# Optimization experiments

Hardware: AMD Instinct MI355X
Metric: run time of the kernel (lower is better)

Reference implementation:

```python
import jax, jax.numpy as jnp
import numpy as np

K = 3          # kernel_size (local window)
PAD = 1        # padding = (K-1)//2 -> 'same' output size
GROUPS = 8
C_OUT = 64


def _unfold3d(x, k):
    """x: [B,C,Dp,Hp,Wp] -> [B,C,D,H,W,kd,kh,kw] sliding windows (stride 1)."""
    B, C, Dp, Hp, Wp = x.shape
    D, H, W = Dp - k + 1, Hp - k + 1, Wp - k + 1
    idx_d = jnp.arange(D)[:, None] + jnp.arange(k)[None, :]
    idx_h = jnp.arange(H)[:, None] + jnp.arange(k)[None, :]
    idx_w = jnp.arange(W)[:, None] + jnp.arange(k)[None, :]
    x = x[:, :, idx_d]              # [B,C,D,kd,Hp,Wp]
    x = x[:, :, :, :, idx_h]        # [B,C,D,kd,H,kh,Wp]
    x = x[:, :, :, :, :, :, idx_w]  # [B,C,D,kd,H,kh,W,kw]
    return jnp.transpose(x, (0, 1, 2, 4, 6, 3, 5, 7))


def setup_inputs() -> dict:
    key = jax.random.key(0)
    ks = jax.random.split(key, 7)
    B, Cin, D, H, W = 1, 64, 16, 64, 64
    c3 = C_OUT // 3                 # 21
    rest = C_OUT - 2 * c3           # 22
    fan_out_scale = np.sqrt(2.0 / C_OUT)  # kaiming_normal fan_out, relu
    x = jax.random.normal(ks[0], (B, Cin, D, H, W), dtype=jnp.float32)
    w_q = jax.random.normal(ks[1], (C_OUT, Cin), dtype=jnp.float32) * fan_out_scale
    w_k = jax.random.normal(ks[2], (C_OUT, Cin), dtype=jnp.float32) * fan_out_scale
    w_v = jax.random.normal(ks[3], (C_OUT, Cin), dtype=jnp.float32) * fan_out_scale
    rel_d = jax.random.normal(ks[4], (c3, 1, 1, 1, K, 1, 1), dtype=jnp.float32)
    rel_h = jax.random.normal(ks[5], (c3, 1, 1, 1, 1, K, 1), dtype=jnp.float32)
    rel_w = jax.random.normal(ks[6], (rest, 1, 1, 1, 1, 1, K), dtype=jnp.float32)
    return {"x": x, "w_q": w_q, "w_k": w_k, "w_v": w_v,
            "rel_d": rel_d, "rel_h": rel_h, "rel_w": rel_w}


def reference(x, w_q, w_k, w_v, rel_d, rel_h, rel_w):
    B, Cin, D, H, W = x.shape
    cg = C_OUT // GROUPS
    c3 = C_OUT // 3
    # 1x1x1 convs (bias=False): plain channel mixing. conv(pad(x)) == pad(conv(x)).
    q = jnp.einsum('oc,bcdhw->bodhw', w_q, x)
    k = jnp.einsum('oc,bcdhw->bodhw', w_k, x)
    v = jnp.einsum('oc,bcdhw->bodhw', w_v, x)
    pad = [(0, 0), (0, 0), (PAD, PAD), (PAD, PAD), (PAD, PAD)]
    k = jnp.pad(k, pad)
    v = jnp.pad(v, pad)
    k_win = _unfold3d(k, K)   # [B,Co,D,H,W,kd,kh,kw]
    v_win = _unfold3d(v, K)
    # split relative position bias across channel thirds
    k_win = jnp.concatenate([
        k_win[:, :c3] + rel_d,
        k_win[:, c3:2 * c3] + rel_h,
        k_win[:, 2 * c3:] + rel_w,
    ], axis=1)
    Kv = K * K * K
    k_win = k_win.reshape(B, GROUPS, cg, D, H, W, Kv)
    v_win = v_win.reshape(B, GROUPS, cg, D, H, W, Kv)
    qg = q.reshape(B, GROUPS, cg, D, H, W, 1)
    attn = jax.nn.softmax(qg * k_win, axis=-1)
    out = jnp.einsum('bncdhwk,bncdhwk->bncdhw', attn, v_win)
    return out.reshape(B, C_OUT, D, H, W)
```

## Files before the change

### kernel.cpp

```cpp
#include <hip/hip_runtime.h>

#define SP    65536
#define DD    16
#define HH    64
#define WW    64
#define CIN   64
#define COUT  64

#define LOG2E 1.44269504f


typedef __attribute__((ext_vector_type(8))) short bf16x8;
typedef __attribute__((ext_vector_type(4))) float f32x4;

__device__ __forceinline__ unsigned short f2bf(float f) {
    const unsigned u = __float_as_uint(f);
    return (unsigned short)((u + 0x7FFFu + ((u >> 16) & 1u)) >> 16);
}
__device__ __forceinline__ float bf2f(unsigned short h) {
    return __uint_as_float((unsigned)h << 16);
}

__global__ __launch_bounds__(256) void proj(const float* __restrict__ x,
                                            const float* __restrict__ wq,
                                            const float* __restrict__ wk,
                                            const float* __restrict__ wv,
                                            float* __restrict__ q,
                                            float* __restrict__ k,
                                            float* __restrict__ v) {
    __shared__ __align__(16) unsigned short xh [64][72];
    __shared__ __align__(16) unsigned short xlo[64][72];
    __shared__ __align__(16) unsigned short wh [64][72];
    __shared__ __align__(16) unsigned short wlo[64][72];

    const int t  = threadIdx.x;
    const int p0 = blockIdx.x * 64;
    const int m  = blockIdx.y;

    const float* __restrict__ wsel = (m == 0) ? wq : (m == 1) ? wk : wv;
    float* __restrict__       osel = (m == 0) ? q  : (m == 1) ? k  : v;

#pragma unroll
    for (int i = 0; i < 2; ++i) {
        const int f  = t + 256 * i;
        const int c2 = (f >> 4) * 2;
        const int jj = f & 15;
        const float4 a = *(const float4*)(x + c2 * SP + p0 + jj * 4);
        const float4 b = *(const float4*)(x + (c2 + 1) * SP + p0 + jj * 4);
        const float* af = (const float*)&a;
        const float* bf = (const float*)&b;
#pragma unroll
        for (int e = 0; e < 4; ++e) {
            const int j = jj * 4 + e;
            const unsigned short ah = f2bf(af[e]);
            const unsigned short bh = f2bf(bf[e]);
            const unsigned short al = f2bf(af[e] - bf2f(ah));
            const unsigned short bl = f2bf(bf[e] - bf2f(bh));
            *(unsigned*)&xh [j][c2] = (unsigned)ah | ((unsigned)bh << 16);
            *(unsigned*)&xlo[j][c2] = (unsigned)al | ((unsigned)bl << 16);
        }
    }
#pragma unroll
    for (int i = 0; i < 4; ++i) {
        const int f  = t + 256 * i;
        const int o  = f >> 4;
        const int jj = f & 15;
        const float4 w4 = *(const float4*)(wsel + o * CIN + jj * 4);
        const float* wf = (const float*)&w4;
        unsigned short h0 = f2bf(wf[0]), h1 = f2bf(wf[1]);
        unsigned short h2 = f2bf(wf[2]), h3 = f2bf(wf[3]);
        unsigned short l0 = f2bf(wf[0] - bf2f(h0)), l1 = f2bf(wf[1] - bf2f(h1));
        unsigned short l2 = f2bf(wf[2] - bf2f(h2)), l3 = f2bf(wf[3] - bf2f(h3));
        *(uint2*)&wh [o][jj * 4] = make_uint2((unsigned)h0 | ((unsigned)h1 << 16),
                                              (unsigned)h2 | ((unsigned)h3 << 16));
        *(uint2*)&wlo[o][jj * 4] = make_uint2((unsigned)l0 | ((unsigned)l1 << 16),
                                              (unsigned)l2 | ((unsigned)l3 << 16));
    }
    __syncthreads();

    const int lane  = t & 63;
    const int wid   = t >> 6;
    const int lo16  = lane & 15;
    const int lg    = lane >> 4;
    const int otile = wid * 16;

    const bf16x8 Ah0 = *(const bf16x8*)&wh [otile + lo16][lg * 8];
    const bf16x8 Ah1 = *(const bf16x8*)&wh [otile + lo16][32 + lg * 8];
    const bf16x8 Al0 = *(const bf16x8*)&wlo[otile + lo16][lg * 8];
    const bf16x8 Al1 = *(const bf16x8*)&wlo[otile + lo16][32 + lg * 8];

    const float scale = (m == 0) ? LOG2E : 1.f;

#pragma unroll
    for (int jt = 0; jt < 4; ++jt) {
        const int jr = jt * 16 + lo16;
        const bf16x8 Bh0 = *(const bf16x8*)&xh [jr][lg * 8];
        const bf16x8 Bl0 = *(const bf16x8*)&xlo[jr][lg * 8];
        const bf16x8 Bh1 = *(const bf16x8*)&xh [jr][32 + lg * 8];
        const bf16x8 Bl1 = *(const bf16x8*)&xlo[jr][32 + lg * 8];
        f32x4 hh = {0.f, 0.f, 0.f, 0.f};
        f32x4 hl = {0.f, 0.f, 0.f, 0.f};
        f32x4 lh = {0.f, 0.f, 0.f, 0.f};
        hh = __builtin_amdgcn_mfma_f32_16x16x32_bf16(Ah0, Bh0, hh, 0, 0, 0);
        hl = __builtin_amdgcn_mfma_f32_16x16x32_bf16(Ah0, Bl0, hl, 0, 0, 0);
        lh = __builtin_amdgcn_mfma_f32_16x16x32_bf16(Al0, Bh0, lh, 0, 0, 0);
        hh = __builtin_amdgcn_mfma_f32_16x16x32_bf16(Ah1, Bh1, hh, 0, 0, 0);
        hl = __builtin_amdgcn_mfma_f32_16x16x32_bf16(Ah1, Bl1, hl, 0, 0, 0);
        lh = __builtin_amdgcn_mfma_f32_16x16x32_bf16(Al1, Bh1, lh, 0, 0, 0);
        float* op = osel + (otile + lg * 4) * SP + p0 + jt * 16 + lo16;
#pragma unroll
        for (int r = 0; r < 4; ++r)
            op[r * SP] = (hh[r] + hl[r] + lh[r]) * scale;
    }
}

__device__ __forceinline__ float dpp_shr1(float x) {
    return __int_as_float(__builtin_amdgcn_mov_dpp(__float_as_int(x), 0x111, 0xf, 0xf, true));
}
__device__ __forceinline__ float dpp_shl1(float x) {
    return __int_as_float(__builtin_amdgcn_mov_dpp(__float_as_int(x), 0x101, 0xf, 0xf, true));
}

template<int AXIS>
__device__ __forceinline__ void attn_walk(const float* __restrict__ kc,
                                          const float* __restrict__ vc,
                                          const float (&ql)[4],
                                          float r0, float r1, float r2,
                                          int wg, int dabs, int habs,
                                          float (&s)[4], float (&a)[4]) {
#pragma unroll 1
    for (int kd = 0; kd < 3; ++kd) {
        const float rdd = (kd == 0) ? r0 : (kd == 1) ? r1 : r2;
        const int dpg   = dabs - 1 + kd;
        const bool okd  = (unsigned)dpg < (unsigned)DD;
#pragma unroll
        for (int kh = 0; kh < 3; ++kh) {
            const float rkh = (kh == 0) ? r0 : (kh == 1) ? r1 : r2;
            const float rr  = (AXIS == 0) ? rdd : rkh;
            const int hpg   = habs - 1 + kh;
            const bool ok   = okd && ((unsigned)hpg < (unsigned)HH);
            const int off   = ok ? ((dpg * HH + hpg) * WW + wg * 4) : 0;
            float4 km = *(const float4*)(kc + off);
            float4 vm = *(const float4*)(vc + off);
            if (!ok) {
                km = make_float4(0.f, 0.f, 0.f, 0.f);
                vm = make_float4(0.f, 0.f, 0.f, 0.f);
            }
            const float kl = dpp_shr1(km.w), kr = dpp_shl1(km.x);
            const float vl = dpp_shr1(vm.w), vr = dpp_shl1(vm.x);
            float krow[6] = { kl, km.x, km.y, km.z, km.w, kr };
            const float vrow[6] = { vl, vm.x, vm.y, vm.z, vm.w, vr };
            if (AXIS != 2) {
#pragma unroll
                for (int j = 0; j < 6; ++j) krow[j] += rr;
            }
#pragma unroll
            for (int wi = 0; wi < 4; ++wi) {
                const float qv = ql[wi];
#pragma unroll
                for (int kw = 0; kw < 3; ++kw) {
                    const float arg = (AXIS == 2)
                                    ? (krow[wi + kw] + ((kw == 0) ? r0 : (kw == 1) ? r1 : r2))
                                    : krow[wi + kw];
                    const float e = __builtin_amdgcn_exp2f(qv * arg);
                    s[wi] += e;
                    a[wi] = fmaf(e, vrow[wi + kw], a[wi]);
                }
            }
        }
    }
}

__global__ __launch_bounds__(256) void attn(const float* __restrict__ kbuf,
                                            const float* __restrict__ vbuf,
                                            const float* __restrict__ qbuf,
                                            const float* __restrict__ rel_d,
                                            const float* __restrict__ rel_h,
                                            const float* __restrict__ rel_w,
                                            float* __restrict__ out) {
    const int dt = blockIdx.x;
    const int ht = blockIdx.y;
    const int o  = blockIdx.z;

    const int d0 = dt * 4;
    const int h0 = ht * 4;
    const int t  = threadIdx.x;

    const float* __restrict__ kc = kbuf + o * SP;
    const float* __restrict__ vc = vbuf + o * SP;

    const int wg = t & 15;
    const int hl = (t >> 4) & 3;
    const int dl = t >> 6;

    const int dabs = d0 + dl;
    const int habs = h0 + hl;

    float ql[4];
    {
        const float4 q4 = *(const float4*)(qbuf + o * SP + (dabs * HH + habs) * WW + wg * 4);
        ql[0] = q4.x; ql[1] = q4.y;
        ql[2] = q4.z; ql[3] = q4.w;
    }

    float s[4] = {};
    float a[4] = {};

    if (o < 21) {
        attn_walk<0>(kc, vc, ql, rel_d[o * 3], rel_d[o * 3 + 1], rel_d[o * 3 + 2],
                     wg, dabs, habs, s, a);
    } else if (o < 42) {
        const int b = o - 21;
        attn_walk<1>(kc, vc, ql, rel_h[b * 3], rel_h[b * 3 + 1], rel_h[b * 3 + 2],
                     wg, dabs, habs, s, a);
    } else {
        const int b = o - 42;
        attn_walk<2>(kc, vc, ql, rel_w[b * 3], rel_w[b * 3 + 1], rel_w[b * 3 + 2],
                     wg, dabs, habs, s, a);
    }

    float4 ov;
    ov.x = a[0] * __builtin_amdgcn_rcpf(s[0]);
    ov.y = a[1] * __builtin_amdgcn_rcpf(s[1]);
    ov.z = a[2] * __builtin_amdgcn_rcpf(s[2]);
    ov.w = a[3] * __builtin_amdgcn_rcpf(s[3]);
    *(float4*)(out + o * SP + (dabs * HH + habs) * WW + wg * 4) = ov;
}

extern "C" void kernel_launch(void* const* d_in, const int* in_sizes, int n_in,
                              void* d_out, int out_size, void* d_ws, size_t ws_size,
                              hipStream_t stream) {
    const float* x     = (const float*)d_in[0];
    const float* w_q   = (const float*)d_in[1];
    const float* w_k   = (const float*)d_in[2];
    const float* w_v   = (const float*)d_in[3];
    const float* rel_d = (const float*)d_in[4];
    const float* rel_h = (const float*)d_in[5];
    const float* rel_w = (const float*)d_in[6];
    float* out = (float*)d_out;

    float* ws = (float*)d_ws;
    float* q  = ws;
    float* k  = ws + (size_t)COUT * SP;
    float* v  = ws + 2 * (size_t)COUT * SP;

    proj<<<dim3(SP / 64, 3), 256, 0, stream>>>(x, w_q, w_k, w_v, q, k, v);
    attn<<<dim3(4, 16, 64), 256, 0, stream>>>(k, v, q, rel_d, rel_h, rel_w, out);
}
```

Baseline: 115.7 us.

## Precompute bf16 hi/lo split of x and weights in a separate kernel

Adds a splitk kernel that converts x into transposed bf16 high/low arrays and the three weight matrices into bf16 high/low pairs once, writing them to workspace. The proj kernel then reads those pre-split operands straight from global memory into MFMA registers, with no LDS staging, no per-block conversion and no barrier. Previously every one of the three projection blocks per tile redid the x split. The cost is an extra kernel launch plus a write and re-read of the bf16 x copies (about the same bytes as the fp32 x), and uncoalesced-ish 16-byte row loads in proj.

After: 136.5 us. 17.9% more time.

```diff
diff --git a/kernel.cpp b/kernel.cpp
--- a/kernel.cpp
+++ b/kernel.cpp
@@ -21,25 +21,44 @@
     return __uint_as_float((unsigned)h << 16);
 }
 
-__global__ __launch_bounds__(256) void proj(const float* __restrict__ x,
-                                            const float* __restrict__ wq,
-                                            const float* __restrict__ wk,
-                                            const float* __restrict__ wv,
-                                            float* __restrict__ q,
-                                            float* __restrict__ k,
-                                            float* __restrict__ v) {
-    __shared__ __align__(16) unsigned short xh [64][72];
-    __shared__ __align__(16) unsigned short xlo[64][72];
-    __shared__ __align__(16) unsigned short wh [64][72];
-    __shared__ __align__(16) unsigned short wlo[64][72];
-
-    const int t  = threadIdx.x;
-    const int p0 = blockIdx.x * 64;
-    const int m  = blockIdx.y;
-
-    const float* __restrict__ wsel = (m == 0) ? wq : (m == 1) ? wk : wv;
-    float* __restrict__       osel = (m == 0) ? q  : (m == 1) ? k  : v;
-
+__global__ __launch_bounds__(256) void splitk(const float* __restrict__ x,
+                                              const float* __restrict__ wq,
+                                              const float* __restrict__ wk,
+                                              const float* __restrict__ wv,
+                                              unsigned short* __restrict__ xhT,
+                                              unsigned short* __restrict__ xlT,
+                                              unsigned short* __restrict__ wsp) {
+    const int bid = blockIdx.x;
+    const int t   = threadIdx.x;
+
+    if (bid >= 1024) {
+        const int m = bid - 1024;
+        const float* __restrict__ wsel = (m == 0) ? wq : (m == 1) ? wk : wv;
+        unsigned short* dh = wsp + m * 8192;
+        unsigned short* dl = dh + 4096;
+#pragma unroll
+        for (int i = 0; i < 4; ++i) {
+            const int f = t + 256 * i;
+            const float4 w4 = *(const float4*)(wsel + f * 4);
+            const float* wf = (const float*)&w4;
+            unsigned short h[4], l[4];
+#pragma unroll
+            for (int e = 0; e < 4; ++e) {
+                h[e] = f2bf(wf[e]);
+                l[e] = f2bf(wf[e] - bf2f(h[e]));
+            }
+            *(uint2*)(dh + f * 4) = make_uint2((unsigned)h[0] | ((unsigned)h[1] << 16),
+                                               (unsigned)h[2] | ((unsigned)h[3] << 16));
+            *(uint2*)(dl + f * 4) = make_uint2((unsigned)l[0] | ((unsigned)l[1] << 16),
+                                               (unsigned)l[2] | ((unsigned)l[3] << 16));
+        }
+        return;
+    }
+
+    __shared__ __align__(16) unsigned short sh[64][72];
+    __shared__ __align__(16) unsigned short sl[64][72];
+
+    const int p0 = bid * 64;
 #pragma unroll
     for (int i = 0; i < 2; ++i) {
         const int f  = t + 256 * i;
@@ -56,48 +75,58 @@
             const unsigned short bh = f2bf(bf[e]);
             const unsigned short al = f2bf(af[e] - bf2f(ah));
             const unsigned short bl = f2bf(bf[e] - bf2f(bh));
-            *(unsigned*)&xh [j][c2] = (unsigned)ah | ((unsigned)bh << 16);
-            *(unsigned*)&xlo[j][c2] = (unsigned)al | ((unsigned)bl << 16);
+            *(unsigned*)&sh[j][c2] = (unsigned)ah | ((unsigned)bh << 16);
+            *(unsigned*)&sl[j][c2] = (unsigned)al | ((unsigned)bl << 16);
         }
     }
+    __syncthreads();
+
 #pragma unroll
     for (int i = 0; i < 4; ++i) {
-        const int f  = t + 256 * i;
-        const int o  = f >> 4;
-        const int jj = f & 15;
-        const float4 w4 = *(const float4*)(wsel + o * CIN + jj * 4);
-        const float* wf = (const float*)&w4;
-        unsigned short h0 = f2bf(wf[0]), h1 = f2bf(wf[1]);
-        unsigned short h2 = f2bf(wf[2]), h3 = f2bf(wf[3]);
-        unsigned short l0 = f2bf(wf[0] - bf2f(h0)), l1 = f2bf(wf[1] - bf2f(h1));
-        unsigned short l2 = f2bf(wf[2] - bf2f(h2)), l3 = f2bf(wf[3] - bf2f(h3));
-        *(uint2*)&wh [o][jj * 4] = make_uint2((unsigned)h0 | ((unsigned)h1 << 16),
-                                              (unsigned)h2 | ((unsigned)h3 << 16));
-        *(uint2*)&wlo[o][jj * 4] = make_uint2((unsigned)l0 | ((unsigned)l1 << 16),
-                                              (unsigned)l2 | ((unsigned)l3 << 16));
-    }
-    __syncthreads();
-
-    const int lane  = t & 63;
-    const int wid   = t >> 6;
+        const int idx = t + 256 * i;
+        const int row = idx >> 4;
+        const int seg = idx & 15;
+        const uint2 hv = *(const uint2*)&sh[row][seg * 4];
+        const uint2 lv = *(const uint2*)&sl[row][seg * 4];
+        *(uint2*)(xhT + (size_t)(p0 + row) * 64 + seg * 4) = hv;
+        *(uint2*)(xlT + (size_t)(p0 + row) * 64 + seg * 4) = lv;
+    }
+}
+
+__global__ __launch_bounds__(256) void proj(const unsigned short* __restrict__ xhT,
+                                            const unsigned short* __restrict__ xlT,
+                                            const unsigned short* __restrict__ wsp,
+                                            float* __restrict__ q,
+                                            float* __restrict__ k,
+                                            float* __restrict__ v) {
+    const int p0 = blockIdx.x * 64;
+    const int m  = blockIdx.y;
+    float* __restrict__ osel = (m == 0) ? q : (m == 1) ? k : v;
+    const unsigned short* wh = wsp + m * 8192;
+    const unsigned short* wl = wh + 4096;
+
+    const int lane  = threadIdx.x & 63;
+    const int wid   = threadIdx.x >> 6;
     const int lo16  = lane & 15;
     const int lg    = lane >> 4;
     const int otile = wid * 16;
 
-    const bf16x8 Ah0 = *(const bf16x8*)&wh [otile + lo16][lg * 8];
-    const bf16x8 Ah1 = *(const bf16x8*)&wh [otile + lo16][32 + lg * 8];
-    const bf16x8 Al0 = *(const bf16x8*)&wlo[otile + lo16][lg * 8];
-    const bf16x8 Al1 = *(const bf16x8*)&wlo[otile + lo16][32 + lg * 8];
+    const bf16x8 Ah0 = *(const bf16x8*)(wh + (otile + lo16) * 64 + lg * 8);
+    const bf16x8 Ah1 = *(const bf16x8*)(wh + (otile + lo16) * 64 + 32 + lg * 8);
+    const bf16x8 Al0 = *(const bf16x8*)(wl + (otile + lo16) * 64 + lg * 8);
+    const bf16x8 Al1 = *(const bf16x8*)(wl + (otile + lo16) * 64 + 32 + lg * 8);
 
     const float scale = (m == 0) ? LOG2E : 1.f;
 
-#pragma unroll
+#pragma unroll 2
     for (int jt = 0; jt < 4; ++jt) {
         const int jr = jt * 16 + lo16;
-        const bf16x8 Bh0 = *(const bf16x8*)&xh [jr][lg * 8];
-        const bf16x8 Bl0 = *(const bf16x8*)&xlo[jr][lg * 8];
-        const bf16x8 Bh1 = *(const bf16x8*)&xh [jr][32 + lg * 8];
-        const bf16x8 Bl1 = *(const bf16x8*)&xlo[jr][32 + lg * 8];
+        const unsigned short* xrh = xhT + (size_t)(p0 + jr) * 64;
+        const unsigned short* xrl = xlT + (size_t)(p0 + jr) * 64;
+        const bf16x8 Bh0 = *(const bf16x8*)(xrh + lg * 8);
+        const bf16x8 Bl0 = *(const bf16x8*)(xrl + lg * 8);
+        const bf16x8 Bh1 = *(const bf16x8*)(xrh + 32 + lg * 8);
+        const bf16x8 Bl1 = *(const bf16x8*)(xrl + 32 + lg * 8);
         f32x4 hh = {0.f, 0.f, 0.f, 0.f};
         f32x4 hl = {0.f, 0.f, 0.f, 0.f};
         f32x4 lh = {0.f, 0.f, 0.f, 0.f};
@@ -243,7 +272,11 @@
     float* q  = ws;
     float* k  = ws + (size_t)COUT * SP;
     float* v  = ws + 2 * (size_t)COUT * SP;
-
-    proj<<<dim3(SP / 64, 3), 256, 0, stream>>>(x, w_q, w_k, w_v, q, k, v);
+    unsigned short* xhT = (unsigned short*)(ws + 3 * (size_t)COUT * SP);
+    unsigned short* xlT = xhT + (size_t)CIN * SP;
+    unsigned short* wsp = xlT + (size_t)CIN * SP;
+
+    splitk<<<dim3(1027), 256, 0, stream>>>(x, w_q, w_k, w_v, xhT, xlT, wsp);
+    proj<<<dim3(SP / 64, 3), 256, 0, stream>>>(xhT, xlT, wsp, q, k, v);
     attn<<<dim3(4, 16, 64), 256, 0, stream>>>(k, v, q, rel_d, rel_h, rel_w, out);
 }
```

## Fuse Q/K/V projections per block and precompute bf16 weight splits

Applied to the files above, without the earlier changes.

Adds a tiny kernel that splits the three weight matrices into bf16 hi/lo parts once into workspace. The projection kernel then runs one block per 64-position tile and computes Q, K and V together, so each x tile is loaded and split into bf16 hi/lo once instead of three times. The cost is one extra launch and more registers for the three weight fragment sets, which may reduce occupancy.

New measurement: 117.6 us. No clear change (+1.6%).

```diff
diff --git a/kernel.cpp b/kernel.cpp
--- a/kernel.cpp
+++ b/kernel.cpp
@@ -21,24 +21,43 @@
     return __uint_as_float((unsigned)h << 16);
 }
 
+__global__ __launch_bounds__(256) void splitw(const float* __restrict__ wq,
+                                              const float* __restrict__ wk,
+                                              const float* __restrict__ wv,
+                                              unsigned short* __restrict__ wsp) {
+    const int m = blockIdx.x;
+    const int t = threadIdx.x;
+    const float* __restrict__ wsel = (m == 0) ? wq : (m == 1) ? wk : wv;
+    unsigned short* dh = wsp + m * 8192;
+    unsigned short* dl = dh + 4096;
+#pragma unroll
+    for (int i = 0; i < 4; ++i) {
+        const int f = t + 256 * i;
+        const float4 w4 = *(const float4*)(wsel + f * 4);
+        const float* wf = (const float*)&w4;
+        unsigned short h[4], l[4];
+#pragma unroll
+        for (int e = 0; e < 4; ++e) {
+            h[e] = f2bf(wf[e]);
+            l[e] = f2bf(wf[e] - bf2f(h[e]));
+        }
+        *(uint2*)(dh + f * 4) = make_uint2((unsigned)h[0] | ((unsigned)h[1] << 16),
+                                           (unsigned)h[2] | ((unsigned)h[3] << 16));
+        *(uint2*)(dl + f * 4) = make_uint2((unsigned)l[0] | ((unsigned)l[1] << 16),
+                                           (unsigned)l[2] | ((unsigned)l[3] << 16));
+    }
+}
+
 __global__ __launch_bounds__(256) void proj(const float* __restrict__ x,
-                                            const float* __restrict__ wq,
-                                            const float* __restrict__ wk,
-                                            const float* __restrict__ wv,
+                                            const unsigned short* __restrict__ wsp,
                                             float* __restrict__ q,
                                             float* __restrict__ k,
                                             float* __restrict__ v) {
     __shared__ __align__(16) unsigned short xh [64][72];
     __shared__ __align__(16) unsigned short xlo[64][72];
-    __shared__ __align__(16) unsigned short wh [64][72];
-    __shared__ __align__(16) unsigned short wlo[64][72];
 
     const int t  = threadIdx.x;
     const int p0 = blockIdx.x * 64;
-    const int m  = blockIdx.y;
-
-    const float* __restrict__ wsel = (m == 0) ? wq : (m == 1) ? wk : wv;
-    float* __restrict__       osel = (m == 0) ? q  : (m == 1) ? k  : v;
 
 #pragma unroll
     for (int i = 0; i < 2; ++i) {
@@ -60,23 +79,6 @@
             *(unsigned*)&xlo[j][c2] = (unsigned)al | ((unsigned)bl << 16);
         }
     }
-#pragma unroll
-    for (int i = 0; i < 4; ++i) {
-        const int f  = t + 256 * i;
-        const int o  = f >> 4;
-        const int jj = f & 15;
-        const float4 w4 = *(const float4*)(wsel + o * CIN + jj * 4);
-        const float* wf = (const float*)&w4;
-        unsigned short h0 = f2bf(wf[0]), h1 = f2bf(wf[1]);
-        unsigned short h2 = f2bf(wf[2]), h3 = f2bf(wf[3]);
-        unsigned short l0 = f2bf(wf[0] - bf2f(h0)), l1 = f2bf(wf[1] - bf2f(h1));
-        unsigned short l2 = f2bf(wf[2] - bf2f(h2)), l3 = f2bf(wf[3] - bf2f(h3));
-        *(uint2*)&wh [o][jj * 4] = make_uint2((unsigned)h0 | ((unsigned)h1 << 16),
-                                              (unsigned)h2 | ((unsigned)h3 << 16));
-        *(uint2*)&wlo[o][jj * 4] = make_uint2((unsigned)l0 | ((unsigned)l1 << 16),
-                                              (unsigned)l2 | ((unsigned)l3 << 16));
-    }
-    __syncthreads();
 
     const int lane  = t & 63;
     const int wid   = t >> 6;
@@ -84,33 +86,45 @@
     const int lg    = lane >> 4;
     const int otile = wid * 16;
 
-    const bf16x8 Ah0 = *(const bf16x8*)&wh [otile + lo16][lg * 8];
-    const bf16x8 Ah1 = *(const bf16x8*)&wh [otile + lo16][32 + lg * 8];
-    const bf16x8 Al0 = *(const bf16x8*)&wlo[otile + lo16][lg * 8];
-    const bf16x8 Al1 = *(const bf16x8*)&wlo[otile + lo16][32 + lg * 8];
-
-    const float scale = (m == 0) ? LOG2E : 1.f;
-
-#pragma unroll
+    bf16x8 Ah[3][2], Al[3][2];
+#pragma unroll
+    for (int m = 0; m < 3; ++m) {
+        const unsigned short* wh = wsp + m * 8192;
+        const unsigned short* wl = wh + 4096;
+#pragma unroll
+        for (int ch = 0; ch < 2; ++ch) {
+            Ah[m][ch] = *(const bf16x8*)(wh + (otile + lo16) * 64 + ch * 32 + lg * 8);
+            Al[m][ch] = *(const bf16x8*)(wl + (otile + lo16) * 64 + ch * 32 + lg * 8);
+        }
+    }
+    __syncthreads();
+
+    float* outp[3] = { q, k, v };
+    const float scl[3] = { LOG2E, 1.f, 1.f };
+
+#pragma unroll 2
     for (int jt = 0; jt < 4; ++jt) {
         const int jr = jt * 16 + lo16;
         const bf16x8 Bh0 = *(const bf16x8*)&xh [jr][lg * 8];
         const bf16x8 Bl0 = *(const bf16x8*)&xlo[jr][lg * 8];
         const bf16x8 Bh1 = *(const bf16x8*)&xh [jr][32 + lg * 8];
         const bf16x8 Bl1 = *(const bf16x8*)&xlo[jr][32 + lg * 8];
-        f32x4 hh = {0.f, 0.f, 0.f, 0.f};
-        f32x4 hl = {0.f, 0.f, 0.f, 0.f};
-        f32x4 lh = {0.f, 0.f, 0.f, 0.f};
-        hh = __builtin_amdgcn_mfma_f32_16x16x32_bf16(Ah0, Bh0, hh, 0, 0, 0);
-        hl = __builtin_amdgcn_mfma_f32_16x16x32_bf16(Ah0, Bl0, hl, 0, 0, 0);
-        lh = __builtin_amdgcn_mfma_f32_16x16x32_bf16(Al0, Bh0, lh, 0, 0, 0);
-        hh = __builtin_amdgcn_mfma_f32_16x16x32_bf16(Ah1, Bh1, hh, 0, 0, 0);
-        hl = __builtin_amdgcn_mfma_f32_16x16x32_bf16(Ah1, Bl1, hl, 0, 0, 0);
-        lh = __builtin_amdgcn_mfma_f32_16x16x32_bf16(Al1, Bh1, lh, 0, 0, 0);
-        float* op = osel + (otile + lg * 4) * SP + p0 + jt * 16 + lo16;
-#pragma unroll
-        for (int r = 0; r < 4; ++r)
-            op[r * SP] = (hh[r] + hl[r] + lh[r]) * scale;
+#pragma unroll
+        for (int m = 0; m < 3; ++m) {
+            f32x4 hh = {0.f, 0.f, 0.f, 0.f};
+            f32x4 hl = {0.f, 0.f, 0.f, 0.f};
+            f32x4 lh = {0.f, 0.f, 0.f, 0.f};
+            hh = __builtin_amdgcn_mfma_f32_16x16x32_bf16(Ah[m][0], Bh0, hh, 0, 0, 0);
+            hl = __builtin_amdgcn_mfma_f32_16x16x32_bf16(Ah[m][0], Bl0, hl, 0, 0, 0);
+            lh = __builtin_amdgcn_mfma_f32_16x16x32_bf16(Al[m][0], Bh0, lh, 0, 0, 0);
+            hh = __builtin_amdgcn_mfma_f32_16x16x32_bf16(Ah[m][1], Bh1, hh, 0, 0, 0);
+            hl = __builtin_amdgcn_mfma_f32_16x16x32_bf16(Ah[m][1], Bl1, hl, 0, 0, 0);
+            lh = __builtin_amdgcn_mfma_f32_16x16x32_bf16(Al[m][1], Bh1, lh, 0, 0, 0);
+            float* op = outp[m] + (otile + lg * 4) * SP + p0 + jt * 16 + lo16;
+#pragma unroll
+            for (int r = 0; r < 4; ++r)
+                op[r * SP] = (hh[r] + hl[r] + lh[r]) * scl[m];
+        }
     }
 }
 
@@ -243,7 +257,9 @@
     float* q  = ws;
     float* k  = ws + (size_t)COUT * SP;
     float* v  = ws + 2 * (size_t)COUT * SP;
-
-    proj<<<dim3(SP / 64, 3), 256, 0, stream>>>(x, w_q, w_k, w_v, q, k, v);
+    unsigned short* wsp = (unsigned short*)(ws + 3 * (size_t)COUT * SP);
+
+    splitw<<<dim3(3), 256, 0, stream>>>(w_q, w_k, w_v, wsp);
+    proj<<<dim3(SP / 64), 256, 0, stream>>>(x, wsp, q, k, v);
     attn<<<dim3(4, 16, 64), 256, 0, stream>>>(k, v, q, rel_d, rel_h, rel_w, out);
 }
```
